# Kernel tuning notes

Hardware: AMD Instinct MI355X
Metric: run time of the kernel (lower is better)

The kernel has to match this reference:

```python
import jax, jax.numpy as jnp
import numpy as np

NEG_INF = -1e38

def wkv(w, u, k, v):
    """Numerically-stable RWKV-4 WKV recurrence.
    w, u: [C] (log-space decay / first-token bonus)
    k, v: [B, T, C]
    returns y: [B, T, C]
    """
    B, T, C = k.shape

    def step(carry, kv):
        p, q, o = carry          # numerator state, denominator state, running log-max; each [B, C]
        kt, vt = kv              # [B, C]
        # output at t (includes the u-boosted current token)
        no = jnp.maximum(o, u + kt)
        A = jnp.exp(o - no)
        Bt = jnp.exp(u + kt - no)
        y = (A * p + Bt * vt) / (A * q + Bt)
        # state update (decay by w, absorb current token)
        no2 = jnp.maximum(w + o, kt)
        A2 = jnp.exp(w + o - no2)
        B2 = jnp.exp(kt - no2)
        return (A2 * p + B2 * vt, A2 * q + B2, no2), y

    init = (jnp.zeros((B, C), k.dtype), jnp.zeros((B, C), k.dtype),
            jnp.full((B, C), NEG_INF, k.dtype))
    kT = jnp.swapaxes(k, 0, 1)   # [T, B, C]
    vT = jnp.swapaxes(v, 0, 1)
    _, ys = jax.lax.scan(step, init, (kT, vT))
    return jnp.swapaxes(ys, 0, 1)


def setup_inputs() -> dict:
    key = jax.random.key(0)
    ks = jax.random.split(key, 10)
    B, T, C = 8, 4096, 512
    scale = 1.0 / np.sqrt(C)
    return {
        "x": jax.random.normal(ks[0], (B, T, C), jnp.float32),
        "spatial_decay": jax.random.normal(ks[1], (C,), jnp.float32),
        "spatial_first": jax.random.normal(ks[2], (C,), jnp.float32),
        "mix_k": jax.random.uniform(ks[3], (1, 1, C), jnp.float32),
        "mix_v": jax.random.uniform(ks[4], (1, 1, C), jnp.float32),
        "mix_r": jax.random.uniform(ks[5], (1, 1, C), jnp.float32),
        "wk": jax.random.normal(ks[6], (C, C), jnp.float32) * scale,
        "wv": jax.random.normal(ks[7], (C, C), jnp.float32) * scale,
        "wr": jax.random.normal(ks[8], (C, C), jnp.float32) * scale,
        "wo": jax.random.normal(ks[9], (C, C), jnp.float32) * scale,
    }


def reference(x, spatial_decay, spatial_first, mix_k, mix_v, mix_r, wk, wv, wr, wo):
    B, T, C = x.shape
    # time_shift: xx[t] = x[t-1], xx[0] = 0  (ZeroPad2d((0,0,1,-1)))
    xx = jnp.pad(x, ((0, 0), (1, 0), (0, 0)))[:, :-1]
    xk = x * mix_k + xx * (1.0 - mix_k)
    xv = x * mix_v + xx * (1.0 - mix_v)
    xr = x * mix_r + xx * (1.0 - mix_r)
    k = jnp.einsum('btc,cd->btd', xk, wk)
    v = jnp.einsum('btc,cd->btd', xv, wv)
    r = jnp.einsum('btc,cd->btd', xr, wr)
    sr = jax.nn.sigmoid(r)
    y = wkv(spatial_decay / T, spatial_first / T, k, v)
    return jnp.einsum('btc,cd->btd', sr * y, wo)
```

## Files before the change

kernel.cpp:

```cpp
#include <hip/hip_runtime.h>

#define BB 8
#define TT 4096
#define CC 512
#define MM (BB * TT)
#define SS 128
#define LL 32

typedef short short8 __attribute__((ext_vector_type(8)));
typedef unsigned short ushort8 __attribute__((ext_vector_type(8)));
typedef float f32x4 __attribute__((ext_vector_type(4)));

__device__ __forceinline__ unsigned short f2bf(float f) {
    unsigned int u = __float_as_uint(f);
    u += 0x7FFFu + ((u >> 16) & 1u);
    return (unsigned short)(u >> 16);
}
__device__ __forceinline__ float bf2f(unsigned short h) {
    return __uint_as_float(((unsigned int)h) << 16);
}

__device__ __forceinline__ void gl_lds16(const void* g, void* l) {
    __builtin_amdgcn_global_load_lds(
        (__attribute__((address_space(1))) void*)(unsigned long long)g,
        (__attribute__((address_space(3))) void*)(unsigned int)(unsigned long long)l,
        16, 0, 0);
}

__device__ __forceinline__ ushort8 pack8(f32x4 a, f32x4 b) {
    ushort8 r;
    r[0] = f2bf(a.x); r[1] = f2bf(a.y); r[2] = f2bf(a.z); r[3] = f2bf(a.w);
    r[4] = f2bf(b.x); r[5] = f2bf(b.y); r[6] = f2bf(b.z); r[7] = f2bf(b.w);
    return r;
}

__global__ void transpose_w(const float* __restrict__ wk, const float* __restrict__ wv,
                            const float* __restrict__ wr, const float* __restrict__ wo,
                            unsigned short* __restrict__ wT) {
    const int which = blockIdx.y;
    const float* src = (which == 0) ? wk : (which == 1) ? wv : (which == 2) ? wr : wo;
    const int i = blockIdx.x * 256 + threadIdx.x;
    const int n = i >> 9;
    const int k = i & 511;
    wT[(size_t)which * (CC * CC) + i] = f2bf(src[(size_t)k * CC + n]);
}

__global__ __launch_bounds__(256) void mix_kvr(
    const float* __restrict__ x,
    const float* __restrict__ mixk, const float* __restrict__ mixv,
    const float* __restrict__ mixr,
    unsigned short* __restrict__ kx, unsigned short* __restrict__ vx,
    unsigned short* __restrict__ rx) {
    const int idx = blockIdx.x * 256 + threadIdx.x;
    const int row = idx >> 6;
    const int ch  = (idx & 63) * 8;
    const int t   = row & (TT - 1);
    const size_t off = (size_t)row * CC + ch;
    const float* xr = x + off;

    const f32x4 zero4 = {0.f, 0.f, 0.f, 0.f};
    const f32x4 one4  = {1.f, 1.f, 1.f, 1.f};

    f32x4 xc0 = ((const f32x4*)xr)[0];
    f32x4 xc1 = ((const f32x4*)xr)[1];
    f32x4 xp0 = zero4, xp1 = zero4;
    if (t != 0) {
        xp0 = ((const f32x4*)(xr - CC))[0];
        xp1 = ((const f32x4*)(xr - CC))[1];
    }

    f32x4 m0, m1;
    m0 = ((const f32x4*)(mixk + ch))[0];
    m1 = ((const f32x4*)(mixk + ch))[1];
    *(ushort8*)(kx + off) = pack8(xc0 * m0 + xp0 * (one4 - m0),
                                  xc1 * m1 + xp1 * (one4 - m1));
    m0 = ((const f32x4*)(mixv + ch))[0];
    m1 = ((const f32x4*)(mixv + ch))[1];
    *(ushort8*)(vx + off) = pack8(xc0 * m0 + xp0 * (one4 - m0),
                                  xc1 * m1 + xp1 * (one4 - m1));
    m0 = ((const f32x4*)(mixr + ch))[0];
    m1 = ((const f32x4*)(mixr + ch))[1];
    *(ushort8*)(rx + off) = pack8(xc0 * m0 + xp0 * (one4 - m0),
                                  xc1 * m1 + xp1 * (one4 - m1));
}

__global__ __launch_bounds__(256, 2) void gemm_kvr(
    const unsigned short* __restrict__ wT,
    unsigned short* __restrict__ kbuf, unsigned short* __restrict__ vbuf,
    unsigned short* __restrict__ srb) {
    __shared__ unsigned short As[64 * 32];
    __shared__ unsigned short Bs[512 * 32];

    const int tid = threadIdx.x;
    const int pm = blockIdx.x, which = blockIdx.y;
    unsigned short* ab = (which == 0) ? kbuf : (which == 1) ? vbuf : srb;
    const unsigned short* wTw = wT + (size_t)which * (CC * CC);

    const int ar  = tid >> 2;
    const int cgs = (tid & 3) ^ ((tid >> 2) & 3);
    const unsigned short* ag = ab + (size_t)(pm * 64 + ar) * CC + cgs * 8;
    unsigned short* al = &As[tid * 8];
    const unsigned short* bgp = wTw + (size_t)ar * CC + cgs * 8;

    const int w = tid >> 6, lane = tid & 63;
    const int q = lane >> 4, l16 = lane & 15;
    const int sw = ((q ^ (l16 & 3))) * 8;

    f32x4 acc[4][8];
#pragma unroll
    for (int i = 0; i < 4; i++)
#pragma unroll
        for (int j = 0; j < 8; j++) acc[i][j] = (f32x4){0.f, 0.f, 0.f, 0.f};

    for (int kt = 0; kt < 16; ++kt) {
        const int k0 = kt * 32;
        gl_lds16(ag + k0, al);
#pragma unroll
        for (int t = 0; t < 8; ++t)
            gl_lds16(bgp + (size_t)t * 64 * CC + k0, &Bs[(t * 256 + tid) * 8]);

        __syncthreads();

        short8 a[4], b[8];
#pragma unroll
        for (int i = 0; i < 4; i++)
            a[i] = *(const short8*)&As[(i * 16 + l16) * 32 + sw];
#pragma unroll
        for (int j = 0; j < 8; j++)
            b[j] = *(const short8*)&Bs[(w * 128 + j * 16 + l16) * 32 + sw];
#pragma unroll
        for (int i = 0; i < 4; i++)
#pragma unroll
            for (int j = 0; j < 8; j++)
                acc[i][j] = __builtin_amdgcn_mfma_f32_16x16x32_bf16(a[i], b[j], acc[i][j], 0, 0, 0);

        __syncthreads();
    }

    const bool sig = (which == 2);
    const size_t rb = (size_t)pm * 64;
#pragma unroll
    for (int i = 0; i < 4; i++)
#pragma unroll
        for (int j = 0; j < 8; j++)
#pragma unroll
            for (int ii = 0; ii < 4; ii++) {
                const int m = i * 16 + q * 4 + ii;
                const int n = w * 128 + j * 16 + l16;
                float val = acc[i][j][ii];
                if (sig) val = 1.0f / (1.0f + __expf(-val));
                ab[(rb + m) * CC + n] = f2bf(val);
            }
}

__global__ __launch_bounds__(256) void wkv_part1(
    const unsigned short* __restrict__ kb, const unsigned short* __restrict__ vb,
    const float* __restrict__ sd,
    float* __restrict__ sp_, float* __restrict__ sq_, float* __restrict__ so_) {
    const int idx = blockIdx.x * 256 + threadIdx.x;
    const int c = idx & (CC - 1);
    const int b = (idx >> 9) & (BB - 1);
    const int s = idx >> 12;
    const float w = sd[c] * (1.0f / (float)TT);
    const size_t base = ((size_t)b * TT + (size_t)s * LL) * CC + c;
    const unsigned short* kp = kb + base;
    const unsigned short* vp = vb + base;

    float p = 0.f, q = 0.f, o = -1e38f;
#pragma unroll 8
    for (int i = 0; i < LL; ++i) {
        const float kt = bf2f(kp[(size_t)i * CC]);
        const float vt = bf2f(vp[(size_t)i * CC]);
        const float no2 = fmaxf(w + o, kt);
        const float A2  = __expf(w + o - no2);
        const float B2  = __expf(kt - no2);
        p = A2 * p + B2 * vt;
        q = A2 * q + B2;
        o = no2;
    }
    sp_[idx] = p; sq_[idx] = q; so_[idx] = o;
}

__global__ __launch_bounds__(256) void wkv_part2(
    const float* __restrict__ sd,
    float* __restrict__ sp_, float* __restrict__ sq_, float* __restrict__ so_) {
    const int idx = blockIdx.x * 256 + threadIdx.x;
    const int c = idx & (CC - 1);
    const float wL = sd[c] * ((float)LL / (float)TT);

    float p = 0.f, q = 0.f, o = -1e38f;
    float lp = sp_[idx], lq = sq_[idx], lo = so_[idx];
    for (int s = 0; s < SS; ++s) {
        const int off = s * (BB * CC) + idx;
        float nlp = 0.f, nlq = 0.f, nlo = 0.f;
        if (s + 1 < SS) {
            nlp = sp_[off + BB * CC];
            nlq = sq_[off + BB * CC];
            nlo = so_[off + BB * CC];
        }
        sp_[off] = p; sq_[off] = q; so_[off] = o;
        const float no = fmaxf(o + wL, lo);
        const float A  = __expf(o + wL - no);
        const float Bc = __expf(lo - no);
        p = A * p + Bc * lp;
        q = A * q + Bc * lq;
        o = no;
        lp = nlp; lq = nlq; lo = nlo;
    }
}

__global__ __launch_bounds__(256) void wkv_part3(
    const unsigned short* __restrict__ kb, const unsigned short* __restrict__ vb,
    const unsigned short* __restrict__ srb,
    const float* __restrict__ sd, const float* __restrict__ sf,
    const float* __restrict__ sp_, const float* __restrict__ sq_,
    const float* __restrict__ so_,
    unsigned short* __restrict__ zb) {
    const int idx = blockIdx.x * 256 + threadIdx.x;
    const int c = idx & (CC - 1);
    const int b = (idx >> 9) & (BB - 1);
    const int s = idx >> 12;
    const float w = sd[c] * (1.0f / (float)TT);
    const float u = sf[c] * (1.0f / (float)TT);
    const size_t base = ((size_t)b * TT + (size_t)s * LL) * CC + c;
    const unsigned short* kp = kb + base;
    const unsigned short* vp = vb + base;
    const unsigned short* sp = srb + base;
    unsigned short* zp = zb + base;

    float p = sp_[idx], q = sq_[idx], o = so_[idx];
#pragma unroll 4
    for (int i = 0; i < LL; ++i) {
        const float kt = bf2f(kp[(size_t)i * CC]);
        const float vt = bf2f(vp[(size_t)i * CC]);
        const float sr = bf2f(sp[(size_t)i * CC]);

        const float no = fmaxf(o, u + kt);
        const float A  = __expf(o - no);
        const float Bt = __expf(u + kt - no);
        const float y  = (A * p + Bt * vt) / (A * q + Bt);
        zp[(size_t)i * CC] = f2bf(sr * y);

        const float no2 = fmaxf(w + o, kt);
        const float A2  = __expf(w + o - no2);
        const float B2  = __expf(kt - no2);
        p = A2 * p + B2 * vt;
        q = A2 * q + B2;
        o = no2;
    }
}

__global__ __launch_bounds__(256, 2) void gemm_out(
    const unsigned short* __restrict__ zb, const unsigned short* __restrict__ woT,
    float* __restrict__ out) {
    __shared__ unsigned short As[128 * 32];
    __shared__ unsigned short Bs[128 * 32];

    const int tid = threadIdx.x;
    const int pm = blockIdx.x, pn = blockIdx.y;

    const int r0 = tid >> 2;
    const int cc = (tid & 3) * 8;
    const unsigned short* ag0 = zb + (size_t)(pm * 128 + r0) * CC + cc;
    const unsigned short* ag1 = ag0 + (size_t)64 * CC;
    const unsigned short* bg0 = woT + (size_t)(pn * 128 + r0) * CC + cc;
    const unsigned short* bg1 = bg0 + (size_t)64 * CC;
    unsigned short* al0 = &As[tid * 8];
    unsigned short* al1 = &As[2048 + tid * 8];
    unsigned short* bl0 = &Bs[tid * 8];
    unsigned short* bl1 = &Bs[2048 + tid * 8];

    const int wave = tid >> 6, lane = tid & 63;
    const int wr_ = wave >> 1, wc_ = wave & 1;
    const int q = lane >> 4, l16 = lane & 15;

    f32x4 acc[4][4];
#pragma unroll
    for (int i = 0; i < 4; i++)
#pragma unroll
        for (int j = 0; j < 4; j++) acc[i][j] = (f32x4){0.f, 0.f, 0.f, 0.f};

    for (int kt = 0; kt < 16; ++kt) {
        const int k0 = kt * 32;
        gl_lds16(ag0 + k0, al0);
        gl_lds16(ag1 + k0, al1);
        gl_lds16(bg0 + k0, bl0);
        gl_lds16(bg1 + k0, bl1);

        __syncthreads();

        short8 a[4], b[4];
#pragma unroll
        for (int i = 0; i < 4; i++)
            a[i] = *(const short8*)&As[(wr_ * 64 + i * 16 + l16) * 32 + q * 8];
#pragma unroll
        for (int j = 0; j < 4; j++)
            b[j] = *(const short8*)&Bs[(wc_ * 64 + j * 16 + l16) * 32 + q * 8];
#pragma unroll
        for (int i = 0; i < 4; i++)
#pragma unroll
            for (int j = 0; j < 4; j++)
                acc[i][j] = __builtin_amdgcn_mfma_f32_16x16x32_bf16(a[i], b[j], acc[i][j], 0, 0, 0);

        __syncthreads();
    }

    const int gm0 = pm * 128 + wr_ * 64;
    const int gn0 = pn * 128 + wc_ * 64;
#pragma unroll
    for (int i = 0; i < 4; i++)
#pragma unroll
        for (int j = 0; j < 4; j++)
#pragma unroll
            for (int ii = 0; ii < 4; ii++) {
                const int m = gm0 + i * 16 + q * 4 + ii;
                const int n = gn0 + j * 16 + l16;
                out[(size_t)m * CC + n] = acc[i][j][ii];
            }
}

extern "C" void kernel_launch(void* const* d_in, const int* in_sizes, int n_in,
                              void* d_out, int out_size, void* d_ws, size_t ws_size,
                              hipStream_t stream) {
    const float* x  = (const float*)d_in[0];
    const float* sd = (const float*)d_in[1];
    const float* sf = (const float*)d_in[2];
    const float* mk = (const float*)d_in[3];
    const float* mv = (const float*)d_in[4];
    const float* mr = (const float*)d_in[5];
    const float* wk = (const float*)d_in[6];
    const float* wv = (const float*)d_in[7];
    const float* wr = (const float*)d_in[8];
    const float* wo = (const float*)d_in[9];
    float* out = (float*)d_out;

    char* ws = (char*)d_ws;
    unsigned short* wT = (unsigned short*)ws;
    unsigned short* kbuf = (unsigned short*)(ws + (size_t)4 * CC * CC * 2);
    unsigned short* vbuf = kbuf + (size_t)MM * CC;
    unsigned short* srb  = vbuf + (size_t)MM * CC;
    unsigned short* zb   = srb + (size_t)MM * CC;
    float* sp_ = (float*)(zb + (size_t)MM * CC);
    float* sq_ = sp_ + (size_t)SS * BB * CC;
    float* so_ = sq_ + (size_t)SS * BB * CC;
    unsigned short* woT = wT + (size_t)3 * CC * CC;

    transpose_w<<<dim3((CC * CC) / 256, 4), 256, 0, stream>>>(wk, wv, wr, wo, wT);

    mix_kvr<<<dim3((MM * CC / 8) / 256), 256, 0, stream>>>(
        x, mk, mv, mr, kbuf, vbuf, srb);

    gemm_kvr<<<dim3(MM / 64, 3), 256, 0, stream>>>(wT, kbuf, vbuf, srb);

    wkv_part1<<<dim3((SS * BB * CC) / 256), 256, 0, stream>>>(kbuf, vbuf, sd, sp_, sq_, so_);
    wkv_part2<<<dim3((BB * CC) / 256), 256, 0, stream>>>(sd, sp_, sq_, so_);
    wkv_part3<<<dim3((SS * BB * CC) / 256), 256, 0, stream>>>(
        kbuf, vbuf, srb, sd, sf, sp_, sq_, so_, zb);

    gemm_out<<<dim3(MM / 128, CC / 128), 256, 0, stream>>>(zb, woT, out);
}
```

Baseline: 329.0 us.

## Retile projection GEMMs to 128x256 with double-buffered LDS and out-of-place outputs

Replaces the in-place 64x512 k/v/r GEMM with a generic 128x256-tile kernel that reads one buffer and writes another, launched separately for each projection. Buffers are rotated so the earlier in-place hazard and its single-stage loop go away. LDS loads are now double-buffered, so the next K slice is fetched while MFMAs run on the current one, with one barrier per step. The output GEMM moves to the same 128x256 double-buffered tiling with a swizzled layout. In exchange it uses more LDS per block and adds two extra kernel launches.

```diff
diff --git a/kernel.cpp b/kernel.cpp
--- a/kernel.cpp
+++ b/kernel.cpp
@@ -84,27 +84,36 @@
                                   xc1 * m1 + xp1 * (one4 - m1));
 }
 
-__global__ __launch_bounds__(256, 2) void gemm_kvr(
-    const unsigned short* __restrict__ wT,
-    unsigned short* __restrict__ kbuf, unsigned short* __restrict__ vbuf,
-    unsigned short* __restrict__ srb) {
-    __shared__ unsigned short As[64 * 32];
-    __shared__ unsigned short Bs[512 * 32];
+#define STAGE_KVR(bufidx, k0) do {                                              \
+    gl_lds16(agA + (k0), &As[bufidx][tid * 8]);                                 \
+    gl_lds16(agA + (size_t)64 * CC + (k0), &As[bufidx][(256 + tid) * 8]);       \
+    _Pragma("unroll")                                                           \
+    for (int s_ = 0; s_ < 4; ++s_)                                              \
+        gl_lds16(agB + (size_t)(s_ * 64) * CC + (k0),                           \
+                 &Bs[bufidx][(s_ * 256 + tid) * 8]);                            \
+} while (0)
+
+__global__ __launch_bounds__(256, 2) void gemm_tile(
+    const unsigned short* __restrict__ A,
+    const unsigned short* __restrict__ Bw,
+    unsigned short* __restrict__ Out,
+    const int sig) {
+    __shared__ unsigned short As[2][128 * 32];
+    __shared__ unsigned short Bs[2][256 * 32];
 
     const int tid = threadIdx.x;
-    const int pm = blockIdx.x, which = blockIdx.y;
-    unsigned short* ab = (which == 0) ? kbuf : (which == 1) ? vbuf : srb;
-    const unsigned short* wTw = wT + (size_t)which * (CC * CC);
-
-    const int ar  = tid >> 2;
-    const int cgs = (tid & 3) ^ ((tid >> 2) & 3);
-    const unsigned short* ag = ab + (size_t)(pm * 64 + ar) * CC + cgs * 8;
-    unsigned short* al = &As[tid * 8];
-    const unsigned short* bgp = wTw + (size_t)ar * CC + cgs * 8;
+    const int pm = blockIdx.x;
+    const int pn = blockIdx.y;
+
+    const int ar = tid >> 2;
+    const int cg = (tid & 3) ^ ((tid >> 3) & 3);
+    const unsigned short* agA = A  + (size_t)(pm * 128 + ar) * CC + cg * 8;
+    const unsigned short* agB = Bw + (size_t)(pn * 256 + ar) * CC + cg * 8;
 
     const int w = tid >> 6, lane = tid & 63;
+    const int wr = w >> 1, wc = w & 1;
     const int q = lane >> 4, l16 = lane & 15;
-    const int sw = ((q ^ (l16 & 3))) * 8;
+    const int sw = (q ^ ((l16 >> 1) & 3)) * 8;
 
     f32x4 acc[4][8];
 #pragma unroll
@@ -112,22 +121,24 @@
 #pragma unroll
         for (int j = 0; j < 8; j++) acc[i][j] = (f32x4){0.f, 0.f, 0.f, 0.f};
 
+    STAGE_KVR(0, 0);
+    __syncthreads();
+
     for (int kt = 0; kt < 16; ++kt) {
-        const int k0 = kt * 32;
-        gl_lds16(ag + k0, al);
-#pragma unroll
-        for (int t = 0; t < 8; ++t)
-            gl_lds16(bgp + (size_t)t * 64 * CC + k0, &Bs[(t * 256 + tid) * 8]);
-
-        __syncthreads();
+        const int cur = kt & 1;
+        if (kt + 1 < 16) {
+            const int nxt = cur ^ 1;
+            const int k0 = (kt + 1) * 32;
+            STAGE_KVR(nxt, k0);
+        }
 
         short8 a[4], b[8];
 #pragma unroll
         for (int i = 0; i < 4; i++)
-            a[i] = *(const short8*)&As[(i * 16 + l16) * 32 + sw];
+            a[i] = *(const short8*)&As[cur][(wr * 64 + i * 16 + l16) * 32 + sw];
 #pragma unroll
         for (int j = 0; j < 8; j++)
-            b[j] = *(const short8*)&Bs[(w * 128 + j * 16 + l16) * 32 + sw];
+            b[j] = *(const short8*)&Bs[cur][(wc * 128 + j * 16 + l16) * 32 + sw];
 #pragma unroll
         for (int i = 0; i < 4; i++)
 #pragma unroll
@@ -137,8 +148,8 @@
         __syncthreads();
     }
 
-    const bool sig = (which == 2);
-    const size_t rb = (size_t)pm * 64;
+    const size_t rb = (size_t)pm * 128 + wr * 64;
+    const int nb = pn * 256 + wc * 128;
 #pragma unroll
     for (int i = 0; i < 4; i++)
 #pragma unroll
@@ -146,10 +157,10 @@
 #pragma unroll
             for (int ii = 0; ii < 4; ii++) {
                 const int m = i * 16 + q * 4 + ii;
-                const int n = w * 128 + j * 16 + l16;
+                const int n = nb + j * 16 + l16;
                 float val = acc[i][j][ii];
                 if (sig) val = 1.0f / (1.0f + __expf(-val));
-                ab[(rb + m) * CC + n] = f2bf(val);
+                Out[(rb + m) * CC + n] = f2bf(val);
             }
 }
 
@@ -253,69 +264,67 @@
 __global__ __launch_bounds__(256, 2) void gemm_out(
     const unsigned short* __restrict__ zb, const unsigned short* __restrict__ woT,
     float* __restrict__ out) {
-    __shared__ unsigned short As[128 * 32];
-    __shared__ unsigned short Bs[128 * 32];
+    __shared__ unsigned short As[2][128 * 32];
+    __shared__ unsigned short Bs[2][256 * 32];
 
     const int tid = threadIdx.x;
-    const int pm = blockIdx.x, pn = blockIdx.y;
-
-    const int r0 = tid >> 2;
-    const int cc = (tid & 3) * 8;
-    const unsigned short* ag0 = zb + (size_t)(pm * 128 + r0) * CC + cc;
-    const unsigned short* ag1 = ag0 + (size_t)64 * CC;
-    const unsigned short* bg0 = woT + (size_t)(pn * 128 + r0) * CC + cc;
-    const unsigned short* bg1 = bg0 + (size_t)64 * CC;
-    unsigned short* al0 = &As[tid * 8];
-    unsigned short* al1 = &As[2048 + tid * 8];
-    unsigned short* bl0 = &Bs[tid * 8];
-    unsigned short* bl1 = &Bs[2048 + tid * 8];
-
-    const int wave = tid >> 6, lane = tid & 63;
-    const int wr_ = wave >> 1, wc_ = wave & 1;
+    const int pm = blockIdx.x;
+    const int pn = blockIdx.y;
+
+    const int ar = tid >> 2;
+    const int cg = (tid & 3) ^ ((tid >> 3) & 3);
+    const unsigned short* agA = zb  + (size_t)(pm * 128 + ar) * CC + cg * 8;
+    const unsigned short* agB = woT + (size_t)(pn * 256 + ar) * CC + cg * 8;
+
+    const int w = tid >> 6, lane = tid & 63;
+    const int wr = w >> 1, wc = w & 1;
     const int q = lane >> 4, l16 = lane & 15;
-
-    f32x4 acc[4][4];
+    const int sw = (q ^ ((l16 >> 1) & 3)) * 8;
+
+    f32x4 acc[4][8];
 #pragma unroll
     for (int i = 0; i < 4; i++)
 #pragma unroll
-        for (int j = 0; j < 4; j++) acc[i][j] = (f32x4){0.f, 0.f, 0.f, 0.f};
+        for (int j = 0; j < 8; j++) acc[i][j] = (f32x4){0.f, 0.f, 0.f, 0.f};
+
+    STAGE_KVR(0, 0);
+    __syncthreads();
 
     for (int kt = 0; kt < 16; ++kt) {
-        const int k0 = kt * 32;
-        gl_lds16(ag0 + k0, al0);
-        gl_lds16(ag1 + k0, al1);
-        gl_lds16(bg0 + k0, bl0);
-        gl_lds16(bg1 + k0, bl1);
+        const int cur = kt & 1;
+        if (kt + 1 < 16) {
+            const int nxt = cur ^ 1;
+            const int k0 = (kt + 1) * 32;
+            STAGE_KVR(nxt, k0);
+        }
+
+        short8 a[4], b[8];
+#pragma unroll
+        for (int i = 0; i < 4; i++)
+            a[i] = *(const short8*)&As[cur][(wr * 64 + i * 16 + l16) * 32 + sw];
+#pragma unroll
+        for (int j = 0; j < 8; j++)
+            b[j] = *(const short8*)&Bs[cur][(wc * 128 + j * 16 + l16) * 32 + sw];
+#pragma unroll
+        for (int i = 0; i < 4; i++)
+#pragma unroll
+            for (int j = 0; j < 8; j++)
+                acc[i][j] = __builtin_amdgcn_mfma_f32_16x16x32_bf16(a[i], b[j], acc[i][j], 0, 0, 0);
 
         __syncthreads();
-
-        short8 a[4], b[4];
-#pragma unroll
-        for (int i = 0; i < 4; i++)
-            a[i] = *(const short8*)&As[(wr_ * 64 + i * 16 + l16) * 32 + q * 8];
-#pragma unroll
-        for (int j = 0; j < 4; j++)
-            b[j] = *(const short8*)&Bs[(wc_ * 64 + j * 16 + l16) * 32 + q * 8];
-#pragma unroll
-        for (int i = 0; i < 4; i++)
-#pragma unroll
-            for (int j = 0; j < 4; j++)
-                acc[i][j] = __builtin_amdgcn_mfma_f32_16x16x32_bf16(a[i], b[j], acc[i][j], 0, 0, 0);
-
-        __syncthreads();
-    }
-
-    const int gm0 = pm * 128 + wr_ * 64;
-    const int gn0 = pn * 128 + wc_ * 64;
+    }
+
+    const size_t rb = (size_t)pm * 128 + wr * 64;
+    const int nb = pn * 256 + wc * 128;
 #pragma unroll
     for (int i = 0; i < 4; i++)
 #pragma unroll
-        for (int j = 0; j < 4; j++)
+        for (int j = 0; j < 8; j++)
 #pragma unroll
             for (int ii = 0; ii < 4; ii++) {
-                const int m = gm0 + i * 16 + q * 4 + ii;
-                const int n = gn0 + j * 16 + l16;
-                out[(size_t)m * CC + n] = acc[i][j][ii];
+                const int m = i * 16 + q * 4 + ii;
+                const int n = nb + j * 16 + l16;
+                out[(rb + m) * CC + n] = acc[i][j][ii];
             }
 }
 
@@ -336,11 +345,11 @@
 
     char* ws = (char*)d_ws;
     unsigned short* wT = (unsigned short*)ws;
-    unsigned short* kbuf = (unsigned short*)(ws + (size_t)4 * CC * CC * 2);
-    unsigned short* vbuf = kbuf + (size_t)MM * CC;
-    unsigned short* srb  = vbuf + (size_t)MM * CC;
-    unsigned short* zb   = srb + (size_t)MM * CC;
-    float* sp_ = (float*)(zb + (size_t)MM * CC);
+    unsigned short* b1 = (unsigned short*)(ws + (size_t)4 * CC * CC * 2);
+    unsigned short* b2 = b1 + (size_t)MM * CC;
+    unsigned short* b3 = b2 + (size_t)MM * CC;
+    unsigned short* b4 = b3 + (size_t)MM * CC;
+    float* sp_ = (float*)(b4 + (size_t)MM * CC);
     float* sq_ = sp_ + (size_t)SS * BB * CC;
     float* so_ = sq_ + (size_t)SS * BB * CC;
     unsigned short* woT = wT + (size_t)3 * CC * CC;
@@ -348,14 +357,16 @@
     transpose_w<<<dim3((CC * CC) / 256, 4), 256, 0, stream>>>(wk, wv, wr, wo, wT);
 
     mix_kvr<<<dim3((MM * CC / 8) / 256), 256, 0, stream>>>(
-        x, mk, mv, mr, kbuf, vbuf, srb);
-
-    gemm_kvr<<<dim3(MM / 64, 3), 256, 0, stream>>>(wT, kbuf, vbuf, srb);
-
-    wkv_part1<<<dim3((SS * BB * CC) / 256), 256, 0, stream>>>(kbuf, vbuf, sd, sp_, sq_, so_);
+        x, mk, mv, mr, b1, b2, b3);
+
+    gemm_tile<<<dim3(MM / 128, 2), 256, 0, stream>>>(b1, wT + (size_t)0 * CC * CC, b4, 0);
+    gemm_tile<<<dim3(MM / 128, 2), 256, 0, stream>>>(b2, wT + (size_t)1 * CC * CC, b1, 0);
+    gemm_tile<<<dim3(MM / 128, 2), 256, 0, stream>>>(b3, wT + (size_t)2 * CC * CC, b2, 1);
+
+    wkv_part1<<<dim3((SS * BB * CC) / 256), 256, 0, stream>>>(b4, b1, sd, sp_, sq_, so_);
     wkv_part2<<<dim3((BB * CC) / 256), 256, 0, stream>>>(sd, sp_, sq_, so_);
     wkv_part3<<<dim3((SS * BB * CC) / 256), 256, 0, stream>>>(
-        kbuf, vbuf, srb, sd, sf, sp_, sq_, so_, zb);
-
-    gemm_out<<<dim3(MM / 128, CC / 128), 256, 0, stream>>>(zb, woT, out);
-}
+        b4, b1, b2, sd, sf, sp_, sq_, so_, b3);
+
+    gemm_out<<<dim3(MM / 128, 2), 256, 0, stream>>>(b3, woT, out);
+}
```

Result: faster. 318.6 us (-3.1%).
